# Kernel optimization log

Measured on AMD Instinct MI355X. Metric: run time of the kernel, lower is better.

Reference implementation:

```python
import jax, jax.numpy as jnp
import numpy as np

B, S, IN_F, OUT_F, R = 4, 4096, 4096, 4096, 1024  # new_r = sqrt((4096+4096)*128) = 1024


def setup_inputs() -> dict:
    key = jax.random.key(0)
    kx, kw, kb, ka = jax.random.split(key, 4)
    x = jax.random.normal(kx, (B, S, IN_F), dtype=jnp.float32)
    W = jax.random.normal(kw, (OUT_F, IN_F), dtype=jnp.float32) * 0.02
    b = jax.random.normal(kb, (OUT_F,), dtype=jnp.float32) * 0.02
    A = jax.random.normal(ka, (R, R), dtype=jnp.float32) * 0.02  # lora_A.weight (init zeros in module; randn here to exercise math)
    return {"x": x, "W": W, "b": b, "A": A}


def reference(x, W, b, A):
    # base linear: y = x @ W.T + b
    result = jnp.einsum('bsi,oi->bso', x, W) + b
    # MoRA adapter, mora_type=1, in_f % r == 0 (no padding needed)
    r = A.shape[0]
    sum_inter = IN_F // r  # 4
    in_x = x.reshape(*x.shape[:-1], sum_inter, r).sum(axis=-2)  # [B,S,r]
    out_x = jnp.einsum('bsr,qr->bsq', in_x, A)  # lora_A(in_x): in_x @ A.T
    repeat_time = -(-OUT_F // r)  # ceil = 4
    out_x = jnp.tile(out_x, (1, 1, repeat_time))[..., :OUT_F]
    return result + out_x
```

## Files before the change

kernel.cpp:

```cpp
#include <hip/hip_runtime.h>
#include <hip/hip_bf16.h>
#include <cstdint>


typedef __attribute__((ext_vector_type(8))) short bf16x8;
typedef __attribute__((ext_vector_type(4))) float f32x4;
typedef __attribute__((ext_vector_type(4))) float fvec4;

static constexpr int MTOT = 16384;
static constexpr int KF   = 4096;
static constexpr int NF   = 4096;
static constexpr int BM = 256, BN = 256, BK = 32;
static constexpr int TILE = BM * BK;
static constexpr int KT = KF / BK;
static constexpr int MB = MTOT / BM;
static constexpr int NB = NF / BN;

__global__ __launch_bounds__(256) void tile_x_kernel(const float* __restrict__ x,
                                                     __hip_bfloat16* __restrict__ xt) {
    int blk = blockIdx.x;
    int mb = blk >> 7, kt = blk & 127;
    int tid = threadIdx.x;
    __hip_bfloat16* dst = xt + (size_t)blk * TILE;
#pragma unroll
    for (int it = 0; it < 4; ++it) {
        int e = (it * 256 + tid) * 8;
        int f = e >> 9;
        int l = (e >> 3) & 63;
        int row = mb * BM + f * 16 + (l & 15);
        int k0  = kt * BK + (l >> 4) * 8;
        const fvec4* s = (const fvec4*)(x + (size_t)row * KF + k0);
        fvec4 v0 = s[0], v1 = s[1];
        union { bf16x8 v; __hip_bfloat16 h[8]; } o;
        o.h[0] = __float2bfloat16(v0[0]); o.h[1] = __float2bfloat16(v0[1]);
        o.h[2] = __float2bfloat16(v0[2]); o.h[3] = __float2bfloat16(v0[3]);
        o.h[4] = __float2bfloat16(v1[0]); o.h[5] = __float2bfloat16(v1[1]);
        o.h[6] = __float2bfloat16(v1[2]); o.h[7] = __float2bfloat16(v1[3]);
        *(bf16x8*)(dst + e) = o.v;
    }
}

__global__ __launch_bounds__(256) void tile_w_kernel(const float* __restrict__ W,
                                                     const float* __restrict__ A,
                                                     __hip_bfloat16* __restrict__ wt) {
    int blk = blockIdx.x;
    int nb = blk >> 7, kt = blk & 127;
    int tid = threadIdx.x;
    __hip_bfloat16* dst = wt + (size_t)blk * TILE;
#pragma unroll
    for (int it = 0; it < 4; ++it) {
        int e = (it * 256 + tid) * 8;
        int f = e >> 9;
        int l = (e >> 3) & 63;
        int o  = nb * BN + f * 16 + (l & 15);
        int k0 = kt * BK + (l >> 4) * 8;
        const fvec4* sw = (const fvec4*)(W + (size_t)o * KF + k0);
        const fvec4* sa = (const fvec4*)(A + (size_t)(o & 1023) * 1024 + (k0 & 1023));
        fvec4 w0 = sw[0], w1 = sw[1];
        fvec4 a0 = sa[0], a1 = sa[1];
        union { bf16x8 v; __hip_bfloat16 h[8]; } ov;
        ov.h[0] = __float2bfloat16(w0[0] + a0[0]); ov.h[1] = __float2bfloat16(w0[1] + a0[1]);
        ov.h[2] = __float2bfloat16(w0[2] + a0[2]); ov.h[3] = __float2bfloat16(w0[3] + a0[3]);
        ov.h[4] = __float2bfloat16(w1[0] + a1[0]); ov.h[5] = __float2bfloat16(w1[1] + a1[1]);
        ov.h[6] = __float2bfloat16(w1[2] + a1[2]); ov.h[7] = __float2bfloat16(w1[3] + a1[7 - 7 + 3]);
        *(bf16x8*)(dst + e) = ov.v;
    }
}

__device__ inline void gload_lds16(const __hip_bfloat16* g, __hip_bfloat16* l) {
    __builtin_amdgcn_global_load_lds(
        (const __attribute__((address_space(1))) unsigned int*)g,
        (__attribute__((address_space(3))) unsigned int*)l, 16, 0, 0);
}

#define STG_A(tt, sl) { const __hip_bfloat16* g = aP + (size_t)(tt) * TILE;      \
    gload_lds16(g, As + (sl) * TILE + t8);                                       \
    gload_lds16(g + 4096, As + (sl) * TILE + 4096 + t8); }
#define STG_B(tt, sl) { const __hip_bfloat16* g = bP + (size_t)(tt) * TILE;      \
    gload_lds16(g, Bs + (sl) * TILE + t8);                                       \
    gload_lds16(g + 4096, Bs + (sl) * TILE + 4096 + t8); }

#define ENDP {                                                                   \
    asm volatile("" ::: "memory");                                               \
    __builtin_amdgcn_s_barrier();                                                \
    asm volatile("" ::: "memory"); }

#define ENDP_W4 {                                                                \
    asm volatile("s_waitcnt vmcnt(4)" ::: "memory");                             \
    __builtin_amdgcn_s_barrier();                                                \
    asm volatile("" ::: "memory"); }

#define PHASE(SL, PH, DOB, STAGE_STMT) {                                         \
    bf16x8 af[4];                                                                \
    {                                                                            \
        const __hip_bfloat16* ab = As + (SL) * TILE + aOff + (PH) * 2048;        \
        af[0] = *(const bf16x8*)(ab);                                            \
        af[1] = *(const bf16x8*)(ab + 512);                                      \
        af[2] = *(const bf16x8*)(ab + 1024);                                     \
        af[3] = *(const bf16x8*)(ab + 1536);                                     \
        if (DOB) {                                                               \
            const __hip_bfloat16* bb = Bs + (SL) * TILE + bOff;                  \
            bfr[0] = *(const bf16x8*)(bb);                                       \
            bfr[1] = *(const bf16x8*)(bb + 512);                                 \
            bfr[2] = *(const bf16x8*)(bb + 1024);                                \
            bfr[3] = *(const bf16x8*)(bb + 1536);                                \
        }                                                                        \
    }                                                                            \
    STAGE_STMT;                                                                  \
    asm volatile("" ::: "memory");                                               \
    __builtin_amdgcn_s_barrier();                                                \
    asm volatile("" ::: "memory");                                               \
    __builtin_amdgcn_s_setprio(1);                                               \
    _Pragma("unroll") for (int m = 0; m < 4; ++m)                                \
        _Pragma("unroll") for (int n = 0; n < 4; ++n)                            \
            acc[(PH) * 4 + m][n] = __builtin_amdgcn_mfma_f32_16x16x32_bf16(      \
                af[m], bfr[n], acc[(PH) * 4 + m][n], 0, 0, 0);                   \
    __builtin_amdgcn_s_setprio(0); }

__global__ __launch_bounds__(512, 2) void gemm_bf16_kernel(
    const __hip_bfloat16* __restrict__ xt, const __hip_bfloat16* __restrict__ wt,
    const float* __restrict__ bias, float* __restrict__ out) {
    extern __shared__ __hip_bfloat16 lds[];
    __hip_bfloat16* As = lds;
    __hip_bfloat16* Bs = lds + 4 * TILE;

    int bid = blockIdx.x;
    int wg = (bid & 7) * 128 + (bid >> 3);
    int nb = wg >> 6;
    int mb = wg & 63;

    int tid = threadIdx.x;
    int lane = tid & 63;
    int wv = tid >> 6;
    int wm = wv >> 2, wn = wv & 3;
    int lr = lane & 15;
    int hi = lane >> 4;
    int t8 = tid * 8;

    int aOff = wm * 4096 + lane * 8;
    int bOff = wn * 2048 + lane * 8;

    const __hip_bfloat16* aP = xt + (size_t)mb * (KT * TILE) + t8;
    const __hip_bfloat16* bP = wt + (size_t)nb * (KT * TILE) + t8;

    f32x4 acc[8][4];
#pragma unroll
    for (int m = 0; m < 8; ++m)
#pragma unroll
        for (int n = 0; n < 4; ++n) acc[m][n] = f32x4{0.f, 0.f, 0.f, 0.f};
    bf16x8 bfr[4];

    STG_A(0, 0); STG_B(0, 0);
    STG_A(1, 1); STG_B(1, 1);
    STG_A(2, 2); STG_B(2, 2);
    ENDP_W4

    for (int j = 0; j < KT / 4; ++j) {
        int tb = 4 * j;
        int t4 = tb + 4; if (t4 >= KT) t4 = 0;
        int t5 = tb + 5; if (t5 >= KT) t5 = 0;
        int t6 = tb + 6; if (t6 >= KT) t6 = 0;
        PHASE(0, 0, 1, STG_A(tb + 3, 3)); ENDP
        PHASE(0, 1, 0, STG_B(tb + 3, 3)); ENDP
        PHASE(1, 0, 1, STG_A(t4, 0));     ENDP
        PHASE(1, 1, 0, STG_B(t4, 0));     ENDP_W4
        PHASE(2, 0, 1, STG_A(t5, 1));     ENDP
        PHASE(2, 1, 0, STG_B(t5, 1));     ENDP
        PHASE(3, 0, 1, STG_A(t6, 2));     ENDP
        PHASE(3, 1, 0, STG_B(t6, 2));     ENDP_W4
    }
    asm volatile("s_waitcnt vmcnt(0)" ::: "memory");

    int row0 = mb * BM + wm * 128;
    int col0 = nb * BN + wn * 64;
#pragma unroll
    for (int n = 0; n < 4; ++n) {
        int col = col0 + n * 16 + lr;
        float bv = bias[col];
#pragma unroll
        for (int mf = 0; mf < 8; ++mf) {
            int row = row0 + mf * 16 + hi * 4;
#pragma unroll
            for (int jj = 0; jj < 4; ++jj)
                out[(size_t)(row + jj) * NF + col] = acc[mf][n][jj] + bv;
        }
    }
}

extern "C" void kernel_launch(void* const* d_in, const int* in_sizes, int n_in,
                              void* d_out, int out_size, void* d_ws, size_t ws_size,
                              hipStream_t stream) {
    const float* x = (const float*)d_in[0];
    const float* W = (const float*)d_in[1];
    const float* b = (const float*)d_in[2];
    const float* A = (const float*)d_in[3];
    float* out = (float*)d_out;

    size_t xt_elems = (size_t)MB * KT * TILE;
    size_t wt_elems = (size_t)NB * KT * TILE;
    size_t need = (xt_elems + wt_elems) * sizeof(__hip_bfloat16);
    if (ws_size < need) return;

    __hip_bfloat16* xt = (__hip_bfloat16*)d_ws;
    __hip_bfloat16* wt = xt + xt_elems;

    (void)hipFuncSetAttribute((const void*)gemm_bf16_kernel,
                              hipFuncAttributeMaxDynamicSharedMemorySize, 131072);

    tile_x_kernel<<<MB * KT, 256, 0, stream>>>(x, xt);
    tile_w_kernel<<<NB * KT, 256, 0, stream>>>(W, A, wt);
    gemm_bf16_kernel<<<MB * NB, 512, 131072, stream>>>(xt, wt, b, out);
}
```

Baseline: 606.4 us.

## Switch GEMM to 32x32x16 MFMA with retiled operand layout and merged phases

Replaces the 16x16x32 bf16 MFMA tiles with 32x32x16 MFMA, re-laying out the pre-tiled x and W+A buffers so each 32-row block holds two 16-wide K halves. The main loop drops from eight half-phases to four full-tile phases, each staging A and B together and waiting with a single vmcnt and barrier. This aims to cut LDS fragment reads per FLOP and the barrier count, but puts more outstanding loads in flight per phase and changes register pressure and the epilogue store pattern.

```diff
diff --git a/kernel.cpp b/kernel.cpp
--- a/kernel.cpp
+++ b/kernel.cpp
@@ -4,7 +4,7 @@
 
 
 typedef __attribute__((ext_vector_type(8))) short bf16x8;
-typedef __attribute__((ext_vector_type(4))) float f32x4;
+typedef __attribute__((ext_vector_type(16))) float f32x16;
 typedef __attribute__((ext_vector_type(4))) float fvec4;
 
 static constexpr int MTOT = 16384;
@@ -27,8 +27,9 @@
         int e = (it * 256 + tid) * 8;
         int f = e >> 9;
         int l = (e >> 3) & 63;
-        int row = mb * BM + f * 16 + (l & 15);
-        int k0  = kt * BK + (l >> 4) * 8;
+        int rb = f >> 1, kh = f & 1;
+        int row = mb * BM + rb * 32 + (l & 31);
+        int k0  = kt * BK + kh * 16 + (l >> 5) * 8;
         const fvec4* s = (const fvec4*)(x + (size_t)row * KF + k0);
         fvec4 v0 = s[0], v1 = s[1];
         union { bf16x8 v; __hip_bfloat16 h[8]; } o;
@@ -52,8 +53,9 @@
         int e = (it * 256 + tid) * 8;
         int f = e >> 9;
         int l = (e >> 3) & 63;
-        int o  = nb * BN + f * 16 + (l & 15);
-        int k0 = kt * BK + (l >> 4) * 8;
+        int rb = f >> 1, kh = f & 1;
+        int o  = nb * BN + rb * 32 + (l & 31);
+        int k0 = kt * BK + kh * 16 + (l >> 5) * 8;
         const fvec4* sw = (const fvec4*)(W + (size_t)o * KF + k0);
         const fvec4* sa = (const fvec4*)(A + (size_t)(o & 1023) * 1024 + (k0 & 1023));
         fvec4 w0 = sw[0], w1 = sw[1];
@@ -62,7 +64,7 @@
         ov.h[0] = __float2bfloat16(w0[0] + a0[0]); ov.h[1] = __float2bfloat16(w0[1] + a0[1]);
         ov.h[2] = __float2bfloat16(w0[2] + a0[2]); ov.h[3] = __float2bfloat16(w0[3] + a0[3]);
         ov.h[4] = __float2bfloat16(w1[0] + a1[0]); ov.h[5] = __float2bfloat16(w1[1] + a1[1]);
-        ov.h[6] = __float2bfloat16(w1[2] + a1[2]); ov.h[7] = __float2bfloat16(w1[3] + a1[7 - 7 + 3]);
+        ov.h[6] = __float2bfloat16(w1[2] + a1[2]); ov.h[7] = __float2bfloat16(w1[3] + a1[3]);
         *(bf16x8*)(dst + e) = ov.v;
     }
 }
@@ -73,49 +75,47 @@
         (__attribute__((address_space(3))) unsigned int*)l, 16, 0, 0);
 }
 
-#define STG_A(tt, sl) { const __hip_bfloat16* g = aP + (size_t)(tt) * TILE;      \
-    gload_lds16(g, As + (sl) * TILE + t8);                                       \
-    gload_lds16(g + 4096, As + (sl) * TILE + 4096 + t8); }
-#define STG_B(tt, sl) { const __hip_bfloat16* g = bP + (size_t)(tt) * TILE;      \
-    gload_lds16(g, Bs + (sl) * TILE + t8);                                       \
-    gload_lds16(g + 4096, Bs + (sl) * TILE + 4096 + t8); }
-
-#define ENDP {                                                                   \
-    asm volatile("" ::: "memory");                                               \
-    __builtin_amdgcn_s_barrier();                                                \
-    asm volatile("" ::: "memory"); }
-
-#define ENDP_W4 {                                                                \
-    asm volatile("s_waitcnt vmcnt(4)" ::: "memory");                             \
-    __builtin_amdgcn_s_barrier();                                                \
-    asm volatile("" ::: "memory"); }
-
-#define PHASE(SL, PH, DOB, STAGE_STMT) {                                         \
-    bf16x8 af[4];                                                                \
+#define STG(tt, sl) { const __hip_bfloat16* ga = aP + (size_t)(tt) * TILE;       \
+    gload_lds16(ga, As + (sl) * TILE + t8);                                      \
+    gload_lds16(ga + 4096, As + (sl) * TILE + 4096 + t8);                        \
+    const __hip_bfloat16* gb = bP + (size_t)(tt) * TILE;                         \
+    gload_lds16(gb, Bs + (sl) * TILE + t8);                                      \
+    gload_lds16(gb + 4096, Bs + (sl) * TILE + 4096 + t8); }
+
+#define PHASE(SL, STAGE_STMT) {                                                  \
+    STAGE_STMT;                                                                  \
+    bf16x8 af[8], bfv[4];                                                        \
     {                                                                            \
-        const __hip_bfloat16* ab = As + (SL) * TILE + aOff + (PH) * 2048;        \
+        const __hip_bfloat16* ab = As + (SL) * TILE + aOff;                      \
         af[0] = *(const bf16x8*)(ab);                                            \
         af[1] = *(const bf16x8*)(ab + 512);                                      \
         af[2] = *(const bf16x8*)(ab + 1024);                                     \
         af[3] = *(const bf16x8*)(ab + 1536);                                     \
-        if (DOB) {                                                               \
-            const __hip_bfloat16* bb = Bs + (SL) * TILE + bOff;                  \
-            bfr[0] = *(const bf16x8*)(bb);                                       \
-            bfr[1] = *(const bf16x8*)(bb + 512);                                 \
-            bfr[2] = *(const bf16x8*)(bb + 1024);                                \
-            bfr[3] = *(const bf16x8*)(bb + 1536);                                \
-        }                                                                        \
+        af[4] = *(const bf16x8*)(ab + 2048);                                     \
+        af[5] = *(const bf16x8*)(ab + 2560);                                     \
+        af[6] = *(const bf16x8*)(ab + 3072);                                     \
+        af[7] = *(const bf16x8*)(ab + 3584);                                     \
+        const __hip_bfloat16* bb = Bs + (SL) * TILE + bOff;                      \
+        bfv[0] = *(const bf16x8*)(bb);                                           \
+        bfv[1] = *(const bf16x8*)(bb + 512);                                     \
+        bfv[2] = *(const bf16x8*)(bb + 1024);                                    \
+        bfv[3] = *(const bf16x8*)(bb + 1536);                                    \
     }                                                                            \
-    STAGE_STMT;                                                                  \
     asm volatile("" ::: "memory");                                               \
     __builtin_amdgcn_s_barrier();                                                \
     asm volatile("" ::: "memory");                                               \
     __builtin_amdgcn_s_setprio(1);                                               \
-    _Pragma("unroll") for (int m = 0; m < 4; ++m)                                \
-        _Pragma("unroll") for (int n = 0; n < 4; ++n)                            \
-            acc[(PH) * 4 + m][n] = __builtin_amdgcn_mfma_f32_16x16x32_bf16(      \
-                af[m], bfr[n], acc[(PH) * 4 + m][n], 0, 0, 0);                   \
-    __builtin_amdgcn_s_setprio(0); }
+    _Pragma("unroll") for (int fm = 0; fm < 4; ++fm)                             \
+        _Pragma("unroll") for (int fn = 0; fn < 2; ++fn) {                       \
+            acc[fm][fn] = __builtin_amdgcn_mfma_f32_32x32x16_bf16(               \
+                af[fm * 2 + 0], bfv[fn * 2 + 0], acc[fm][fn], 0, 0, 0);          \
+            acc[fm][fn] = __builtin_amdgcn_mfma_f32_32x32x16_bf16(               \
+                af[fm * 2 + 1], bfv[fn * 2 + 1], acc[fm][fn], 0, 0, 0);          \
+        }                                                                        \
+    __builtin_amdgcn_s_setprio(0);                                               \
+    asm volatile("s_waitcnt vmcnt(8)" ::: "memory");                             \
+    __builtin_amdgcn_s_barrier();                                                \
+    asm volatile("" ::: "memory"); }
 
 __global__ __launch_bounds__(512, 2) void gemm_bf16_kernel(
     const __hip_bfloat16* __restrict__ xt, const __hip_bfloat16* __restrict__ wt,
@@ -133,8 +133,6 @@
     int lane = tid & 63;
     int wv = tid >> 6;
     int wm = wv >> 2, wn = wv & 3;
-    int lr = lane & 15;
-    int hi = lane >> 4;
     int t8 = tid * 8;
 
     int aOff = wm * 4096 + lane * 8;
@@ -143,46 +141,47 @@
     const __hip_bfloat16* aP = xt + (size_t)mb * (KT * TILE) + t8;
     const __hip_bfloat16* bP = wt + (size_t)nb * (KT * TILE) + t8;
 
-    f32x4 acc[8][4];
-#pragma unroll
-    for (int m = 0; m < 8; ++m)
-#pragma unroll
-        for (int n = 0; n < 4; ++n) acc[m][n] = f32x4{0.f, 0.f, 0.f, 0.f};
-    bf16x8 bfr[4];
-
-    STG_A(0, 0); STG_B(0, 0);
-    STG_A(1, 1); STG_B(1, 1);
-    STG_A(2, 2); STG_B(2, 2);
-    ENDP_W4
+    f32x16 acc[4][2];
+#pragma unroll
+    for (int fm = 0; fm < 4; ++fm)
+#pragma unroll
+        for (int fn = 0; fn < 2; ++fn)
+#pragma unroll
+            for (int r = 0; r < 16; ++r) acc[fm][fn][r] = 0.f;
+
+    STG(0, 0); STG(1, 1); STG(2, 2);
+    asm volatile("s_waitcnt vmcnt(8)" ::: "memory");
+    __builtin_amdgcn_s_barrier();
+    asm volatile("" ::: "memory");
 
     for (int j = 0; j < KT / 4; ++j) {
         int tb = 4 * j;
         int t4 = tb + 4; if (t4 >= KT) t4 = 0;
         int t5 = tb + 5; if (t5 >= KT) t5 = 0;
         int t6 = tb + 6; if (t6 >= KT) t6 = 0;
-        PHASE(0, 0, 1, STG_A(tb + 3, 3)); ENDP
-        PHASE(0, 1, 0, STG_B(tb + 3, 3)); ENDP
-        PHASE(1, 0, 1, STG_A(t4, 0));     ENDP
-        PHASE(1, 1, 0, STG_B(t4, 0));     ENDP_W4
-        PHASE(2, 0, 1, STG_A(t5, 1));     ENDP
-        PHASE(2, 1, 0, STG_B(t5, 1));     ENDP
-        PHASE(3, 0, 1, STG_A(t6, 2));     ENDP
-        PHASE(3, 1, 0, STG_B(t6, 2));     ENDP_W4
+        PHASE(0, STG(tb + 3, 3));
+        PHASE(1, STG(t4, 0));
+        PHASE(2, STG(t5, 1));
+        PHASE(3, STG(t6, 2));
     }
     asm volatile("s_waitcnt vmcnt(0)" ::: "memory");
 
     int row0 = mb * BM + wm * 128;
     int col0 = nb * BN + wn * 64;
-#pragma unroll
-    for (int n = 0; n < 4; ++n) {
-        int col = col0 + n * 16 + lr;
+    int ln31 = lane & 31;
+    int l5 = lane >> 5;
+#pragma unroll
+    for (int fn = 0; fn < 2; ++fn) {
+        int col = col0 + fn * 32 + ln31;
         float bv = bias[col];
 #pragma unroll
-        for (int mf = 0; mf < 8; ++mf) {
-            int row = row0 + mf * 16 + hi * 4;
-#pragma unroll
-            for (int jj = 0; jj < 4; ++jj)
-                out[(size_t)(row + jj) * NF + col] = acc[mf][n][jj] + bv;
+        for (int fm = 0; fm < 4; ++fm) {
+            int rbase = row0 + fm * 32 + 4 * l5;
+#pragma unroll
+            for (int r = 0; r < 16; ++r) {
+                int row = rbase + (r & 3) + 8 * (r >> 2);
+                out[(size_t)row * NF + col] = acc[fm][fn][r] + bv;
+            }
         }
     }
 }
```

Result: slower. 627.3 us (+3.4%).

## Restructure bf16 GEMM main loop to BK=64 with half-tile staging and double buffering

Applied to the files above, without the earlier changes.

Raises the K tile from 32 to 64 and reorganizes the pre-tiled bf16 layout into 128-row halves. The main loop moves from a 4-slot ring of BK=32 tiles to two 64-wide LDS buffers, with A and B staged at different lookaheads. Each barrier-delimited phase now issues twice as many MFMAs between barriers, cutting barrier and loop overhead per unit of work. The cost is a shallower prefetch in slots, more fragment registers live (Af[8], two B sets), and new scheduling barriers that constrain the compiler.

```diff
diff --git a/kernel.cpp b/kernel.cpp
--- a/kernel.cpp
+++ b/kernel.cpp
@@ -10,32 +10,35 @@
 static constexpr int MTOT = 16384;
 static constexpr int KF   = 4096;
 static constexpr int NF   = 4096;
-static constexpr int BM = 256, BN = 256, BK = 32;
-static constexpr int TILE = BM * BK;
+static constexpr int BM = 256, BN = 256, BK = 64;
 static constexpr int KT = KF / BK;
+static constexpr int HALF = 128 * 64;
 static constexpr int MB = MTOT / BM;
 static constexpr int NB = NF / BN;
+
 
 __global__ __launch_bounds__(256) void tile_x_kernel(const float* __restrict__ x,
                                                      __hip_bfloat16* __restrict__ xt) {
     int blk = blockIdx.x;
-    int mb = blk >> 7, kt = blk & 127;
+    int mb = blk >> 7;
+    int r  = blk & 127;
+    int kt = r >> 1, h = r & 1;
     int tid = threadIdx.x;
-    __hip_bfloat16* dst = xt + (size_t)blk * TILE;
+    __hip_bfloat16* dst = xt + (size_t)blk * HALF;
 #pragma unroll
     for (int it = 0; it < 4; ++it) {
         int e = (it * 256 + tid) * 8;
-        int f = e >> 9;
+        int g = e >> 9;
         int l = (e >> 3) & 63;
-        int row = mb * BM + f * 16 + (l & 15);
-        int k0  = kt * BK + (l >> 4) * 8;
+        int row = mb * BM + h * 128 + (g >> 1) * 16 + (l & 15);
+        int k0  = kt * BK + (g & 1) * 32 + (l >> 4) * 8;
         const fvec4* s = (const fvec4*)(x + (size_t)row * KF + k0);
         fvec4 v0 = s[0], v1 = s[1];
-        union { bf16x8 v; __hip_bfloat16 h[8]; } o;
-        o.h[0] = __float2bfloat16(v0[0]); o.h[1] = __float2bfloat16(v0[1]);
-        o.h[2] = __float2bfloat16(v0[2]); o.h[3] = __float2bfloat16(v0[3]);
-        o.h[4] = __float2bfloat16(v1[0]); o.h[5] = __float2bfloat16(v1[1]);
-        o.h[6] = __float2bfloat16(v1[2]); o.h[7] = __float2bfloat16(v1[3]);
+        union { bf16x8 v; __hip_bfloat16 hh[8]; } o;
+        o.hh[0] = __float2bfloat16(v0[0]); o.hh[1] = __float2bfloat16(v0[1]);
+        o.hh[2] = __float2bfloat16(v0[2]); o.hh[3] = __float2bfloat16(v0[3]);
+        o.hh[4] = __float2bfloat16(v1[0]); o.hh[5] = __float2bfloat16(v1[1]);
+        o.hh[6] = __float2bfloat16(v1[2]); o.hh[7] = __float2bfloat16(v1[3]);
         *(bf16x8*)(dst + e) = o.v;
     }
 }
@@ -44,25 +47,27 @@
                                                      const float* __restrict__ A,
                                                      __hip_bfloat16* __restrict__ wt) {
     int blk = blockIdx.x;
-    int nb = blk >> 7, kt = blk & 127;
+    int nb = blk >> 7;
+    int r  = blk & 127;
+    int kt = r >> 1, h = r & 1;
     int tid = threadIdx.x;
-    __hip_bfloat16* dst = wt + (size_t)blk * TILE;
+    __hip_bfloat16* dst = wt + (size_t)blk * HALF;
 #pragma unroll
     for (int it = 0; it < 4; ++it) {
         int e = (it * 256 + tid) * 8;
-        int f = e >> 9;
+        int g = e >> 9;
         int l = (e >> 3) & 63;
-        int o  = nb * BN + f * 16 + (l & 15);
-        int k0 = kt * BK + (l >> 4) * 8;
+        int o  = nb * BN + h * 128 + (g >> 1) * 16 + (l & 15);
+        int k0 = kt * BK + (g & 1) * 32 + (l >> 4) * 8;
         const fvec4* sw = (const fvec4*)(W + (size_t)o * KF + k0);
         const fvec4* sa = (const fvec4*)(A + (size_t)(o & 1023) * 1024 + (k0 & 1023));
         fvec4 w0 = sw[0], w1 = sw[1];
         fvec4 a0 = sa[0], a1 = sa[1];
-        union { bf16x8 v; __hip_bfloat16 h[8]; } ov;
-        ov.h[0] = __float2bfloat16(w0[0] + a0[0]); ov.h[1] = __float2bfloat16(w0[1] + a0[1]);
-        ov.h[2] = __float2bfloat16(w0[2] + a0[2]); ov.h[3] = __float2bfloat16(w0[3] + a0[3]);
-        ov.h[4] = __float2bfloat16(w1[0] + a1[0]); ov.h[5] = __float2bfloat16(w1[1] + a1[1]);
-        ov.h[6] = __float2bfloat16(w1[2] + a1[2]); ov.h[7] = __float2bfloat16(w1[3] + a1[7 - 7 + 3]);
+        union { bf16x8 v; __hip_bfloat16 hh[8]; } ov;
+        ov.hh[0] = __float2bfloat16(w0[0] + a0[0]); ov.hh[1] = __float2bfloat16(w0[1] + a0[1]);
+        ov.hh[2] = __float2bfloat16(w0[2] + a0[2]); ov.hh[3] = __float2bfloat16(w0[3] + a0[3]);
+        ov.hh[4] = __float2bfloat16(w1[0] + a1[0]); ov.hh[5] = __float2bfloat16(w1[1] + a1[1]);
+        ov.hh[6] = __float2bfloat16(w1[2] + a1[2]); ov.hh[7] = __float2bfloat16(w1[3] + a1[3]);
         *(bf16x8*)(dst + e) = ov.v;
     }
 }
@@ -73,56 +78,67 @@
         (__attribute__((address_space(3))) unsigned int*)l, 16, 0, 0);
 }
 
-#define STG_A(tt, sl) { const __hip_bfloat16* g = aP + (size_t)(tt) * TILE;      \
-    gload_lds16(g, As + (sl) * TILE + t8);                                       \
-    gload_lds16(g + 4096, As + (sl) * TILE + 4096 + t8); }
-#define STG_B(tt, sl) { const __hip_bfloat16* g = bP + (size_t)(tt) * TILE;      \
-    gload_lds16(g, Bs + (sl) * TILE + t8);                                       \
-    gload_lds16(g + 4096, Bs + (sl) * TILE + 4096 + t8); }
-
-#define ENDP {                                                                   \
-    asm volatile("" ::: "memory");                                               \
-    __builtin_amdgcn_s_barrier();                                                \
+#define STG_A(u, h, d) { const __hip_bfloat16* g_ = aP + (size_t)((u) * 2 + (h)) * HALF + t8; \
+    __hip_bfloat16* l_ = As + ((d) * 2 + (h)) * HALF + t8;                        \
+    gload_lds16(g_, l_); gload_lds16(g_ + 4096, l_ + 4096); }
+#define STG_B(u, h, d) { const __hip_bfloat16* g_ = bP + (size_t)((u) * 2 + (h)) * HALF + t8; \
+    __hip_bfloat16* l_ = Bs + ((d) * 2 + (h)) * HALF + t8;                        \
+    gload_lds16(g_, l_); gload_lds16(g_ + 4096, l_ + 4096); }
+
+#define RD_A(d, mq) { const __hip_bfloat16* p_ = As + ((d) * 2 + wm) * HALF + (mq) * 4096 + lane8; \
+    Af[0] = *(const bf16x8*)(p_);        Af[1] = *(const bf16x8*)(p_ + 512);      \
+    Af[2] = *(const bf16x8*)(p_ + 1024); Af[3] = *(const bf16x8*)(p_ + 1536);     \
+    Af[4] = *(const bf16x8*)(p_ + 2048); Af[5] = *(const bf16x8*)(p_ + 2560);     \
+    Af[6] = *(const bf16x8*)(p_ + 3072); Af[7] = *(const bf16x8*)(p_ + 3584); }
+#define RD_B(dst, d, nq) { const __hip_bfloat16* p_ = Bs + ((d) * 2 + bh) * HALF + bn + (nq) * 2048 + lane8; \
+    dst[0] = *(const bf16x8*)(p_);        dst[1] = *(const bf16x8*)(p_ + 512);    \
+    dst[2] = *(const bf16x8*)(p_ + 1024); dst[3] = *(const bf16x8*)(p_ + 1536); }
+
+#define BAR_IN {                                                                  \
+    asm volatile("" ::: "memory");                                                \
+    __builtin_amdgcn_s_barrier();                                                 \
+    __builtin_amdgcn_sched_barrier(0); }
+
+#define BAR_OUT {                                                                 \
+    asm volatile("" ::: "memory");                                                \
+    __builtin_amdgcn_s_barrier();                                                 \
     asm volatile("" ::: "memory"); }
 
-#define ENDP_W4 {                                                                \
-    asm volatile("s_waitcnt vmcnt(4)" ::: "memory");                             \
-    __builtin_amdgcn_s_barrier();                                                \
+#define BAR_OUT_V4 {                                                              \
+    asm volatile("s_waitcnt vmcnt(4)" ::: "memory");                              \
+    __builtin_amdgcn_s_barrier();                                                 \
     asm volatile("" ::: "memory"); }
 
-#define PHASE(SL, PH, DOB, STAGE_STMT) {                                         \
-    bf16x8 af[4];                                                                \
-    {                                                                            \
-        const __hip_bfloat16* ab = As + (SL) * TILE + aOff + (PH) * 2048;        \
-        af[0] = *(const bf16x8*)(ab);                                            \
-        af[1] = *(const bf16x8*)(ab + 512);                                      \
-        af[2] = *(const bf16x8*)(ab + 1024);                                     \
-        af[3] = *(const bf16x8*)(ab + 1536);                                     \
-        if (DOB) {                                                               \
-            const __hip_bfloat16* bb = Bs + (SL) * TILE + bOff;                  \
-            bfr[0] = *(const bf16x8*)(bb);                                       \
-            bfr[1] = *(const bf16x8*)(bb + 512);                                 \
-            bfr[2] = *(const bf16x8*)(bb + 1024);                                \
-            bfr[3] = *(const bf16x8*)(bb + 1536);                                \
-        }                                                                        \
-    }                                                                            \
-    STAGE_STMT;                                                                  \
-    asm volatile("" ::: "memory");                                               \
-    __builtin_amdgcn_s_barrier();                                                \
-    asm volatile("" ::: "memory");                                               \
-    __builtin_amdgcn_s_setprio(1);                                               \
-    _Pragma("unroll") for (int m = 0; m < 4; ++m)                                \
-        _Pragma("unroll") for (int n = 0; n < 4; ++n)                            \
-            acc[(PH) * 4 + m][n] = __builtin_amdgcn_mfma_f32_16x16x32_bf16(      \
-                af[m], bfr[n], acc[(PH) * 4 + m][n], 0, 0, 0);                   \
+#define MM(mq, nq, BF) {                                                          \
+    __builtin_amdgcn_s_setprio(1);                                                \
+    _Pragma("unroll") for (int m = 0; m < 4; ++m)                                 \
+        _Pragma("unroll") for (int n = 0; n < 2; ++n) {                           \
+            acc[(mq) * 4 + m][(nq) * 2 + n] = __builtin_amdgcn_mfma_f32_16x16x32_bf16( \
+                Af[m * 2 + 0], BF[n * 2 + 0], acc[(mq) * 4 + m][(nq) * 2 + n], 0, 0, 0); \
+            acc[(mq) * 4 + m][(nq) * 2 + n] = __builtin_amdgcn_mfma_f32_16x16x32_bf16( \
+                Af[m * 2 + 1], BF[n * 2 + 1], acc[(mq) * 4 + m][(nq) * 2 + n], 0, 0, 0); \
+        }                                                                         \
     __builtin_amdgcn_s_setprio(0); }
+
+#define TILE64(u, d) {                                                            \
+    RD_A(d, 0) RD_B(Bf0, d, 0)                                                    \
+    STG_A(((u) + 1) & 63, 0, (d) ^ 1)                                             \
+    BAR_IN  MM(0, 0, Bf0) BAR_OUT                                                 \
+    RD_B(Bf1, d, 1)                                                               \
+    STG_A(((u) + 1) & 63, 1, (d) ^ 1)                                             \
+    BAR_IN  MM(0, 1, Bf1) BAR_OUT                                                 \
+    RD_A(d, 1)                                                                    \
+    STG_B(((u) + 2) & 63, 0, d)                                                   \
+    BAR_IN  MM(1, 0, Bf0) BAR_OUT                                                 \
+    STG_B(((u) + 2) & 63, 1, d)                                                   \
+    BAR_IN  MM(1, 1, Bf1) BAR_OUT_V4 }
 
 __global__ __launch_bounds__(512, 2) void gemm_bf16_kernel(
     const __hip_bfloat16* __restrict__ xt, const __hip_bfloat16* __restrict__ wt,
     const float* __restrict__ bias, float* __restrict__ out) {
     extern __shared__ __hip_bfloat16 lds[];
     __hip_bfloat16* As = lds;
-    __hip_bfloat16* Bs = lds + 4 * TILE;
+    __hip_bfloat16* Bs = lds + 32768;
 
     int bid = blockIdx.x;
     int wg = (bid & 7) * 128 + (bid >> 3);
@@ -133,56 +149,47 @@
     int lane = tid & 63;
     int wv = tid >> 6;
     int wm = wv >> 2, wn = wv & 3;
+    int bh = wn >> 1;
+    int bn = (wn & 1) * 4096;
+    int lane8 = lane * 8;
+    int t8 = tid * 8;
+
+    const __hip_bfloat16* aP = xt + (size_t)mb * (KT * 2 * HALF);
+    const __hip_bfloat16* bP = wt + (size_t)nb * (KT * 2 * HALF);
+
+    f32x4 acc[8][4];
+#pragma unroll
+    for (int mf = 0; mf < 8; ++mf)
+#pragma unroll
+        for (int nf = 0; nf < 4; ++nf) acc[mf][nf] = f32x4{0.f, 0.f, 0.f, 0.f};
+    bf16x8 Af[8], Bf0[4], Bf1[4];
+
+    STG_A(0, 0, 0) STG_A(0, 1, 0) STG_B(0, 0, 0) STG_B(0, 1, 0)
+    STG_B(1, 0, 1) STG_B(1, 1, 1)
+    asm volatile("s_waitcnt vmcnt(4)" ::: "memory");
+    __builtin_amdgcn_s_barrier();
+    asm volatile("" ::: "memory");
+
+    for (int uu = 0; uu < KT; uu += 2) {
+        TILE64(uu, 0)
+        TILE64(uu + 1, 1)
+    }
+    asm volatile("s_waitcnt vmcnt(0)" ::: "memory");
+
+    int row0 = mb * BM + wm * 128;
+    int col0 = nb * BN + wn * 64;
     int lr = lane & 15;
     int hi = lane >> 4;
-    int t8 = tid * 8;
-
-    int aOff = wm * 4096 + lane * 8;
-    int bOff = wn * 2048 + lane * 8;
-
-    const __hip_bfloat16* aP = xt + (size_t)mb * (KT * TILE) + t8;
-    const __hip_bfloat16* bP = wt + (size_t)nb * (KT * TILE) + t8;
-
-    f32x4 acc[8][4];
-#pragma unroll
-    for (int m = 0; m < 8; ++m)
-#pragma unroll
-        for (int n = 0; n < 4; ++n) acc[m][n] = f32x4{0.f, 0.f, 0.f, 0.f};
-    bf16x8 bfr[4];
-
-    STG_A(0, 0); STG_B(0, 0);
-    STG_A(1, 1); STG_B(1, 1);
-    STG_A(2, 2); STG_B(2, 2);
-    ENDP_W4
-
-    for (int j = 0; j < KT / 4; ++j) {
-        int tb = 4 * j;
-        int t4 = tb + 4; if (t4 >= KT) t4 = 0;
-        int t5 = tb + 5; if (t5 >= KT) t5 = 0;
-        int t6 = tb + 6; if (t6 >= KT) t6 = 0;
-        PHASE(0, 0, 1, STG_A(tb + 3, 3)); ENDP
-        PHASE(0, 1, 0, STG_B(tb + 3, 3)); ENDP
-        PHASE(1, 0, 1, STG_A(t4, 0));     ENDP
-        PHASE(1, 1, 0, STG_B(t4, 0));     ENDP_W4
-        PHASE(2, 0, 1, STG_A(t5, 1));     ENDP
-        PHASE(2, 1, 0, STG_B(t5, 1));     ENDP
-        PHASE(3, 0, 1, STG_A(t6, 2));     ENDP
-        PHASE(3, 1, 0, STG_B(t6, 2));     ENDP_W4
-    }
-    asm volatile("s_waitcnt vmcnt(0)" ::: "memory");
-
-    int row0 = mb * BM + wm * 128;
-    int col0 = nb * BN + wn * 64;
-#pragma unroll
-    for (int n = 0; n < 4; ++n) {
-        int col = col0 + n * 16 + lr;
+#pragma unroll
+    for (int nf = 0; nf < 4; ++nf) {
+        int col = col0 + nf * 16 + lr;
         float bv = bias[col];
 #pragma unroll
         for (int mf = 0; mf < 8; ++mf) {
             int row = row0 + mf * 16 + hi * 4;
 #pragma unroll
             for (int jj = 0; jj < 4; ++jj)
-                out[(size_t)(row + jj) * NF + col] = acc[mf][n][jj] + bv;
+                out[(size_t)(row + jj) * NF + col] = acc[mf][nf][jj] + bv;
         }
     }
 }
@@ -196,8 +203,8 @@
     const float* A = (const float*)d_in[3];
     float* out = (float*)d_out;
 
-    size_t xt_elems = (size_t)MB * KT * TILE;
-    size_t wt_elems = (size_t)NB * KT * TILE;
+    size_t xt_elems = (size_t)MB * KT * 2 * HALF;
+    size_t wt_elems = (size_t)NB * KT * 2 * HALF;
     size_t need = (xt_elems + wt_elems) * sizeof(__hip_bfloat16);
     if (ws_size < need) return;
 
@@ -207,7 +214,7 @@
     (void)hipFuncSetAttribute((const void*)gemm_bf16_kernel,
                               hipFuncAttributeMaxDynamicSharedMemorySize, 131072);
 
-    tile_x_kernel<<<MB * KT, 256, 0, stream>>>(x, xt);
-    tile_w_kernel<<<NB * KT, 256, 0, stream>>>(W, A, wt);
+    tile_x_kernel<<<MB * KT * 2, 256, 0, stream>>>(x, xt);
+    tile_w_kernel<<<NB * KT * 2, 256, 0, stream>>>(W, A, wt);
     gemm_bf16_kernel<<<MB * NB, 512, 131072, stream>>>(xt, wt, b, out);
 }
```

After: 587.4 us. -3.1%, faster.
